# Performance work log

Measured on AMD Instinct MI355X. Metric: run time of the kernel, lower is better.

## Reference

```python
import jax, jax.numpy as jnp
import numpy as np

NMS_THRESH = 0.4          # used as both iou_threshold and score_threshold (as in source)
VAR0, VAR1 = 0.1, 0.2     # variances
MAX_OUT = 200             # max_output_size hardcoded in source
N_ANCHORS = 172032        # 2*(256^2+128^2+64^2), strides 8/16/32 on 2048x2048


def _decode(cls_pred, reg_pred, lnd_pred, anchors):
    # scores: prob of face class (column 1)
    scores = cls_pred.reshape(-1, 2)[:, 1]
    reg = reg_pred.reshape(-1, 4) * jnp.array([VAR0, VAR0, VAR1, VAR1], dtype=reg_pred.dtype)
    dx, dy, dw, dh = reg[:, 0], reg[:, 1], reg[:, 2], reg[:, 3]
    x_a, y_a, w_a, h_a = anchors[:, 0], anchors[:, 1], anchors[:, 2], anchors[:, 3]
    xc = dx * w_a + x_a
    yc = dy * h_a + y_a
    w = jnp.exp(dw) * w_a
    h = jnp.exp(dh) * h_a
    # boxes in [ymin, xmin, ymax, xmax] (tf.image.non_max_suppression convention)
    boxes = jnp.stack([yc - h / 2, xc - w / 2, yc + h / 2, xc + w / 2], axis=1)
    lnd = lnd_pred.reshape(-1, 5, 2) * VAR0
    lx = lnd[..., 0] * w_a[:, None] + x_a[:, None]
    ly = lnd[..., 1] * h_a[:, None] + y_a[:, None]
    lnd10 = jnp.stack([lx, ly], axis=-1).reshape(-1, 10)
    return boxes, scores, lnd10


def _nms(boxes, scores):
    # Greedy NMS, fixed MAX_OUT iterations; invalid slots flagged False.
    y1, x1, y2, x2 = boxes[:, 0], boxes[:, 1], boxes[:, 2], boxes[:, 3]
    areas = (y2 - y1) * (x2 - x1)
    s0 = jnp.where(scores > NMS_THRESH, scores, -jnp.inf)  # score_threshold

    def step(s, _):
        i = jnp.argmax(s)
        valid = s[i] > -jnp.inf
        b = boxes[i]  # (4,) = [iy1, ix1, iy2, ix2]
        ih = jnp.maximum(jnp.minimum(y2, b[2]) - jnp.maximum(y1, b[0]), 0.0)
        iw = jnp.maximum(jnp.minimum(x2, b[3]) - jnp.maximum(x1, b[1]), 0.0)
        inter = ih * iw
        iou = inter / (areas + areas[i] - inter + 1e-12)
        # selected box has IoU 1 with itself -> suppressed too
        s = jnp.where(valid & (iou > NMS_THRESH), -jnp.inf, s)
        return s, (i, valid)

    _, (idxs, valids) = jax.lax.scan(step, s0, None, length=MAX_OUT)
    return idxs, valids


def setup_inputs() -> dict:
    key = jax.random.key(0)
    k1, k2, k3, k4 = jax.random.split(key, 4)
    N = N_ANCHORS
    cls_pred = jax.random.normal(k1, (N, 2), jnp.float32)
    reg_pred = jax.random.normal(k2, (N, 4), jnp.float32) * 0.5
    lnd_pred = jax.random.normal(k3, (N, 10), jnp.float32) * 0.5
    centers = jax.random.uniform(k4, (N, 2), jnp.float32)  # normalized anchor centers
    wh = jnp.full((N, 2), 0.05, jnp.float32)               # anchor widths/heights
    anchors = jnp.concatenate([centers, wh], axis=1)       # [N,4] = (xc, yc, w, h)
    return {"cls_pred": cls_pred, "reg_pred": reg_pred, "lnd_pred": lnd_pred, "anchors": anchors}


def reference(cls_pred, reg_pred, lnd_pred, anchors):
    boxes, scores, lnd10 = _decode(cls_pred, reg_pred, lnd_pred, anchors)
    idxs, valids = _nms(boxes, scores)
    m = valids.astype(boxes.dtype)[:, None]
    # fixed-shape padded outputs: invalid rows zeroed (tf returns variable length)
    return boxes[idxs] * m, lnd10[idxs] * m
```

## Files before the change

kernel.cpp:

```cpp
#include <hip/hip_runtime.h>
#include <stdint.h>

#pragma clang fp contract(off)

#define N_ANCHORS 172032
#define MAX_OUT 200
#define BLK 1024
#define GRID 168
#define NW (BLK / 64)
#define SEG 32
#define NKEY (GRID * SEG)
#define RMAX 1024
#define MASKW (RMAX / 64)
#define MBLK 256
#define MROWS 16
#define RCAND 64
#define RGRID (NKEY / RCAND)
#define RBLK 512
#define RW (RBLK / 64)
#define VT 2.35f

typedef unsigned long long ull;
static_assert(GRID * BLK == N_ANCHORS, "grid covers anchors exactly");
static_assert(RMAX % 64 == 0, "mask words");
static_assert(RGRID * RCAND == NKEY, "rank grid covers key capacity");
static_assert(GRID <= 192, "prefix scan uses 3 waves");

__device__ __forceinline__ void decode_box_d(const float4* __restrict__ reg,
                                             const float4* __restrict__ anc, int i,
                                             double b[4]) {
#pragma clang fp contract(off)
    float4 r = reg[i];
    float4 a = anc[i];
    double dx = (double)r.x * 0.1;
    double dy = (double)r.y * 0.1;
    double dw = (double)r.z * 0.2;
    double dh = (double)r.w * 0.2;
    double xa = (double)a.x, ya = (double)a.y, wa = (double)a.z, ha = (double)a.w;
    double xc = dx * wa; xc = xc + xa;
    double yc = dy * ha; yc = yc + ya;
    double w = exp(dw) * wa;
    double h = exp(dh) * ha;
    double h2 = h * 0.5, w2 = w * 0.5;
    b[0] = yc - h2; b[1] = xc - w2; b[2] = yc + h2; b[3] = xc + w2;
}

__device__ __forceinline__ void write_row(const float4* __restrict__ reg,
                                          const float4* __restrict__ anc,
                                          const float* __restrict__ lnd,
                                          int q, int idx, float* __restrict__ out) {
#pragma clang fp contract(off)
    float b[4] = {0.f, 0.f, 0.f, 0.f};
    float l10[10] = {0.f, 0.f, 0.f, 0.f, 0.f, 0.f, 0.f, 0.f, 0.f, 0.f};
    if (idx >= 0) {
        double bb[4];
        decode_box_d(reg, anc, idx, bb);
        b[0] = (float)bb[0]; b[1] = (float)bb[1]; b[2] = (float)bb[2]; b[3] = (float)bb[3];
        float4 a = anc[idx];
        double xa = (double)a.x, ya = (double)a.y, wa = (double)a.z, ha = (double)a.w;
        for (int j = 0; j < 5; ++j) {
            double lx = (double)lnd[idx * 10 + 2 * j]     * 0.1;
            double ly = (double)lnd[idx * 10 + 2 * j + 1] * 0.1;
            lx = lx * wa; lx = lx + xa;
            ly = ly * ha; ly = ly + ya;
            l10[2 * j] = (float)lx; l10[2 * j + 1] = (float)ly;
        }
    }
    for (int c = 0; c < 4; ++c)  out[q * 4 + c] = b[c];
    for (int c = 0; c < 10; ++c) out[MAX_OUT * 4 + q * 10 + c] = l10[c];
}

__device__ __forceinline__ ull wmax(ull k) {
    for (int d = 32; d > 0; d >>= 1) {
        ull o = __shfl_down(k, d, 64);
        if (o > k) k = o;
    }
    return k;
}

__device__ __forceinline__ ull readlane64(ull v, int l) {
    unsigned lo = (unsigned)__builtin_amdgcn_readlane((int)(unsigned)(v & 0xffffffffull), l);
    unsigned hi = (unsigned)__builtin_amdgcn_readlane((int)(unsigned)(v >> 32), l);
    return ((ull)hi << 32) | (ull)lo;
}

__device__ __forceinline__ bool iou_gt_f4(float4 a, float4 p) {
#pragma clang fp contract(off)
    double y1 = (double)a.x, x1 = (double)a.y, y2 = (double)a.z, x2 = (double)a.w;
    double p0 = (double)p.x, p1 = (double)p.y, p2 = (double)p.z, p3 = (double)p.w;
    double ih = fmin(y2, p2) - fmax(y1, p0); ih = fmax(ih, 0.0);
    double iw = fmin(x2, p3) - fmax(x1, p1); iw = fmax(iw, 0.0);
    double inter = ih * iw;
    double aj = (y2 - y1) * (x2 - x1);
    double ap = (p2 - p0) * (p3 - p1);
    double den = aj + ap; den = den - inter; den = den + 1e-12;
    return (inter / den) > 0.4;
}

__global__ void __launch_bounds__(BLK) k_seg(const float2* __restrict__ cls,
                                             int* __restrict__ segcnt,
                                             ull* __restrict__ segkeys) {
    __shared__ int wcnt[NW];
    int tid = threadIdx.x, bid = blockIdx.x;
    int i = bid * BLK + tid;
    float sc = cls[i].y;
    bool c = (sc > VT);
    ull key = 0ull;
    if (c) key = ((ull)__float_as_uint(sc) << 32)
               | (ull)(0xFFFFFFFFu - (unsigned int)i);
    ull m = __ballot(c);
    int wid = tid >> 6, lane = tid & 63;
    if (lane == 0) wcnt[wid] = __popcll(m);
    __syncthreads();
    if (tid == 0) {
        int s = 0;
        for (int w = 0; w < NW; ++w) { int t = wcnt[w]; wcnt[w] = s; s += t; }
        segcnt[bid] = s;
    }
    __syncthreads();
    if (c) {
        int pos = wcnt[wid] + __popcll(m & ((1ull << lane) - 1ull));
        if (pos < SEG) segkeys[bid * SEG + pos] = key;
    }
}

__device__ __forceinline__ void rank_emit(const float4* __restrict__ reg,
                                          const float4* __restrict__ anc,
                                          int rank, ull key,
                                          int* __restrict__ gidx,
                                          float4* __restrict__ gbox) {
    int idx = (int)(0xFFFFFFFFu - (unsigned int)key);
    gidx[rank] = idx;
    double b[4];
    decode_box_d(reg, anc, idx, b);
    gbox[rank] = make_float4((float)b[0], (float)b[1], (float)b[2], (float)b[3]);
}

__global__ void __launch_bounds__(RBLK) k_rank(const float4* __restrict__ reg,
                                               const float4* __restrict__ anc,
                                               const int* __restrict__ segcnt,
                                               const ull* __restrict__ segkeys,
                                               int* __restrict__ meta,
                                               int* __restrict__ gidx,
                                               float4* __restrict__ gbox) {
    __shared__ ull skeys[NKEY];
    __shared__ int scnt[GRID], spre[GRID];
    __shared__ int wsum[4];
    __shared__ ull wovf[4];
    __shared__ int spart[RBLK];
    __shared__ int s_ok, s_csel;
    int tid = threadIdx.x, wid = tid >> 6, lane = tid & 63;

    int v = 0; bool ovf = false;
    if (tid < GRID) { v = segcnt[tid]; scnt[tid] = v; ovf = (v > SEG); }
    int x = v;
    for (int d = 1; d < 64; d <<= 1) {
        int o = __shfl_up(x, d, 64);
        if (lane >= d) x += o;
    }
    ull om = __ballot(ovf);
    if (wid < 3 && lane == 63) { wsum[wid] = x; wovf[wid] = om; }
    __syncthreads();
    if (tid == 0) {
        int total = wsum[0] + wsum[1] + wsum[2];
        s_csel = total;
        s_ok = ((wovf[0] | wovf[1] | wovf[2]) == 0ull) ? 1 : 0;
        if (blockIdx.x == 0) { meta[0] = s_ok; meta[1] = total; }
    }
    __syncthreads();
    if (tid < GRID)
        spre[tid] = (x - v) + (wid >= 1 ? wsum[0] : 0) + (wid >= 2 ? wsum[1] : 0);
    bool okl = (s_ok != 0);
    int csel = s_csel;
    int cbase = blockIdx.x * RCAND;
    __syncthreads();
    if (!okl) return;
    if (cbase >= csel) return;

    for (int t = tid; t < GRID * SEG; t += RBLK) {
        int s = t >> 5, k = t & (SEG - 1);
        if (k < scnt[s]) skeys[spre[s] + k] = segkeys[t];
    }
    __syncthreads();

    int per = (csel + RW - 1) / RW;
    int jb = wid * per;
    int je = jb + per; if (je > csel) je = csel;
    int c = cbase + lane;
    ull kc = (c < csel) ? skeys[c] : 0ull;
    int rk = 0;
#pragma unroll 8
    for (int j = jb; j < je; ++j)
        rk += (skeys[j] > kc) ? 1 : 0;
    spart[wid * 64 + lane] = rk;
    __syncthreads();

    if (tid < RCAND) {
        int cc = cbase + tid;
        if (cc < csel) {
            int r = 0;
#pragma unroll
            for (int w = 0; w < RW; ++w) r += spart[w * 64 + tid];
            if (r < RMAX) rank_emit(reg, anc, r, skeys[cc], gidx, gbox);
        }
    }
}

__global__ void __launch_bounds__(MBLK) k_mask(const int* __restrict__ meta,
                                               const float4* __restrict__ gbox,
                                               ull* __restrict__ gmask) {
    __shared__ float4 cbox[RMAX];
    if (meta[0] == 0) return;
    int csel = meta[1];
    int rlim = csel < RMAX ? csel : RMAX;
    int tid = threadIdx.x;
    for (int t = tid; t < RMAX; t += MBLK) cbox[t] = gbox[t];
    __syncthreads();
    int row  = blockIdx.x * MROWS + (tid & (MROWS - 1));
    int word = tid >> 4;
    if (row >= rlim) return;
    float4 br = cbox[row];
    ull bits = 0ull;
    int cbase = word << 6;
#pragma unroll 4
    for (int e = 0; e < 64; ++e) {
        int c = cbase + e;
        if (c < rlim && iou_gt_f4(cbox[c], br)) bits |= (1ull << e);
    }
    gmask[row * MASKW + word] = bits;
}

__global__ void __launch_bounds__(BLK) k_pick(const float2* __restrict__ cls,
                                              const float4* __restrict__ reg,
                                              const float4* __restrict__ anc,
                                              const float* __restrict__ lnd,
                                              const int* __restrict__ meta,
                                              const int* __restrict__ gidx,
                                              const ull* __restrict__ gmask,
                                              float* __restrict__ sbuf,
                                              float* __restrict__ out) {
    __shared__ __align__(16) ull smask[RMAX * MASKW];
    __shared__ int s_kept[MAX_OUT];
    __shared__ int s_ln;
    __shared__ ull warr[NW];
    __shared__ ull s_win;
    __shared__ double s_pb[5];

    int tid = threadIdx.x;
    bool pre_ok = (meta[0] != 0);
    int csel = meta[1];
    int ln = 0;

    if (pre_ok) {
        int rlim = csel < RMAX ? csel : RMAX;
        int nv4 = rlim * (MASKW / 2);
        const float4* gm4 = (const float4*)gmask;
        float4* sm4 = (float4*)smask;
        for (int t = tid; t < nv4; t += BLK) sm4[t] = gm4[t];
        __syncthreads();
        if (tid < 64) {
            int lane = tid;
            ull alive = 0ull;
            if (lane < MASKW) {
                int lo = lane << 6;
                int n = rlim - lo;
                if (n >= 64) alive = ~0ull;
                else if (n > 0) alive = (1ull << n) - 1ull;
            }
            int lnl = 0;
            while (lnl < MAX_OUT) {
                ull bal = __ballot(alive != 0ull);
                if (bal == 0ull) break;
                int wl = __ffsll(bal) - 1;
                ull aw = readlane64(alive, wl);
                int bit = __ffsll(aw) - 1;
                int p = (wl << 6) + bit;
                if (lane == 0) s_kept[lnl] = p;
                lnl++;
                ull rw = (lane < MASKW) ? smask[p * MASKW + lane] : 0ull;
                alive &= ~rw;
            }
            if (lane == 0) s_ln = lnl;
        }
        __syncthreads();
        ln = s_ln;
    }

    bool need = (!pre_ok) || (ln < MAX_OUT);
    if (!need) {
        if (tid < MAX_OUT) write_row(reg, anc, lnd, tid, gidx[s_kept[tid]], out);
        return;
    }

    for (int i = tid; i < N_ANCHORS; i += BLK) {
        float sc = cls[i].y;
        sbuf[i] = ((double)sc > 0.4) ? sc : 0.0f;
    }
    __syncthreads();
    ln = 0;
    for (int oi = 0; oi < MAX_OUT; ++oi) {
        ull k = 0;
        for (int i = tid; i < N_ANCHORS; i += BLK) {
            ull kk = ((ull)__float_as_uint(sbuf[i]) << 32)
                   | (ull)(0xFFFFFFFFu - (unsigned int)i);
            if (kk > k) k = kk;
        }
        k = wmax(k);
        if ((tid & 63) == 0) warr[tid >> 6] = k;
        __syncthreads();
        if (tid < 64) {
            ull v = (tid < NW) ? warr[tid] : 0ull;
            v = wmax(v);
            if (tid == 0) s_win = v;
        }
        __syncthreads();
        ull win = s_win;
        if ((win >> 32) == 0u) break;
        int pidx = (int)(0xFFFFFFFFu - (unsigned int)win);
        if (tid == 0) {
            double b[4];
            decode_box_d(reg, anc, pidx, b);
            s_pb[0] = b[0]; s_pb[1] = b[1]; s_pb[2] = b[2]; s_pb[3] = b[3];
            s_pb[4] = (b[2] - b[0]) * (b[3] - b[1]);
            s_kept[oi] = pidx;
        }
        __syncthreads();
        double p0 = s_pb[0], p1 = s_pb[1], p2 = s_pb[2], p3 = s_pb[3], pa = s_pb[4];
        for (int i = tid; i < N_ANCHORS; i += BLK) {
            float v = sbuf[i];
            if (v != 0.0f) {
                double b[4];
                decode_box_d(reg, anc, i, b);
                double ih = fmin(b[2], p2) - fmax(b[0], p0); ih = fmax(ih, 0.0);
                double iw = fmin(b[3], p3) - fmax(b[1], p1); iw = fmax(iw, 0.0);
                double inter = ih * iw;
                double aa = (b[2] - b[0]) * (b[3] - b[1]);
                double den = aa + pa; den = den - inter; den = den + 1e-12;
                if (inter / den > 0.4) sbuf[i] = 0.0f;
            }
        }
        __syncthreads();
        ln = oi + 1;
    }
    __syncthreads();
    if (tid < MAX_OUT)
        write_row(reg, anc, lnd, tid, (tid < ln) ? s_kept[tid] : -1, out);
}

extern "C" void kernel_launch(void* const* d_in, const int* in_sizes, int n_in,
                              void* d_out, int out_size, void* d_ws, size_t ws_size,
                              hipStream_t stream) {
    const float2* cls = (const float2*)d_in[0];
    const float4* reg = (const float4*)d_in[1];
    const float*  lnd = (const float*)d_in[2];
    const float4* anc = (const float4*)d_in[3];

    uint8_t* w = (uint8_t*)d_ws;
    int*    segcnt  = (int*)w;
    int*    meta    = (int*)(w + 768);
    ull*    segkeys = (ull*)(w + 1024);
    int*    gidx    = (int*)(w + 44032);
    float4* gbox    = (float4*)(w + 48128);
    ull*    gmask   = (ull*)(w + 64512);
    float*  sbuf    = (float*)(w + 44032);

    k_seg <<<GRID, BLK, 0, stream>>>(cls, segcnt, segkeys);
    k_rank<<<RGRID, RBLK, 0, stream>>>(reg, anc, segcnt, segkeys, meta, gidx, gbox);
    k_mask<<<RMAX / MROWS, MBLK, 0, stream>>>(meta, gbox, gmask);
    k_pick<<<1, BLK, 0, stream>>>(cls, reg, anc, lnd, meta, gidx, gmask, sbuf,
                                  (float*)d_out);
}
```

Measured before the change: 116.2 us.

## Fuse four NMS kernels into one cooperative kernel with grid syncs

New measurement: 292.7 us. 152% more time.

```diff
diff --git a/kernel.cpp b/kernel.cpp
--- a/kernel.cpp
+++ b/kernel.cpp
@@ -1,5 +1,8 @@
 #include <hip/hip_runtime.h>
+#include <hip/hip_cooperative_groups.h>
 #include <stdint.h>
+
+namespace cg = cooperative_groups;
 
 #pragma clang fp contract(off)
 
@@ -12,18 +15,14 @@
 #define NKEY (GRID * SEG)
 #define RMAX 1024
 #define MASKW (RMAX / 64)
-#define MBLK 256
-#define MROWS 16
-#define RCAND 64
-#define RGRID (NKEY / RCAND)
-#define RBLK 512
-#define RW (RBLK / 64)
+#define RCAND 32
+#define NSLICE 32
 #define VT 2.35f
 
 typedef unsigned long long ull;
 static_assert(GRID * BLK == N_ANCHORS, "grid covers anchors exactly");
 static_assert(RMAX % 64 == 0, "mask words");
-static_assert(RGRID * RCAND == NKEY, "rank grid covers key capacity");
+static_assert(GRID * RCAND == NKEY, "rank grid covers key capacity");
 static_assert(GRID <= 192, "prefix scan uses 3 waves");
 
 __device__ __forceinline__ void decode_box_d(const float4* __restrict__ reg,
@@ -50,24 +49,28 @@
                                           const float* __restrict__ lnd,
                                           int q, int idx, float* __restrict__ out) {
 #pragma clang fp contract(off)
-    float b[4] = {0.f, 0.f, 0.f, 0.f};
-    float l10[10] = {0.f, 0.f, 0.f, 0.f, 0.f, 0.f, 0.f, 0.f, 0.f, 0.f};
+    float4 bv = make_float4(0.f, 0.f, 0.f, 0.f);
+    float2 lv[5];
+    for (int j = 0; j < 5; ++j) lv[j] = make_float2(0.f, 0.f);
     if (idx >= 0) {
         double bb[4];
         decode_box_d(reg, anc, idx, bb);
-        b[0] = (float)bb[0]; b[1] = (float)bb[1]; b[2] = (float)bb[2]; b[3] = (float)bb[3];
+        bv = make_float4((float)bb[0], (float)bb[1], (float)bb[2], (float)bb[3]);
         float4 a = anc[idx];
         double xa = (double)a.x, ya = (double)a.y, wa = (double)a.z, ha = (double)a.w;
+        const float2* l2p = (const float2*)lnd;
         for (int j = 0; j < 5; ++j) {
-            double lx = (double)lnd[idx * 10 + 2 * j]     * 0.1;
-            double ly = (double)lnd[idx * 10 + 2 * j + 1] * 0.1;
+            float2 lp = l2p[idx * 5 + j];
+            double lx = (double)lp.x * 0.1;
+            double ly = (double)lp.y * 0.1;
             lx = lx * wa; lx = lx + xa;
             ly = ly * ha; ly = ly + ya;
-            l10[2 * j] = (float)lx; l10[2 * j + 1] = (float)ly;
-        }
-    }
-    for (int c = 0; c < 4; ++c)  out[q * 4 + c] = b[c];
-    for (int c = 0; c < 10; ++c) out[MAX_OUT * 4 + q * 10 + c] = l10[c];
+            lv[j] = make_float2((float)lx, (float)ly);
+        }
+    }
+    *(float4*)&out[q * 4] = bv;
+    float2* o2 = (float2*)&out[MAX_OUT * 4 + q * 10];
+    for (int j = 0; j < 5; ++j) o2[j] = lv[j];
 }
 
 __device__ __forceinline__ ull wmax(ull k) {
@@ -97,33 +100,6 @@
     return (inter / den) > 0.4;
 }
 
-__global__ void __launch_bounds__(BLK) k_seg(const float2* __restrict__ cls,
-                                             int* __restrict__ segcnt,
-                                             ull* __restrict__ segkeys) {
-    __shared__ int wcnt[NW];
-    int tid = threadIdx.x, bid = blockIdx.x;
-    int i = bid * BLK + tid;
-    float sc = cls[i].y;
-    bool c = (sc > VT);
-    ull key = 0ull;
-    if (c) key = ((ull)__float_as_uint(sc) << 32)
-               | (ull)(0xFFFFFFFFu - (unsigned int)i);
-    ull m = __ballot(c);
-    int wid = tid >> 6, lane = tid & 63;
-    if (lane == 0) wcnt[wid] = __popcll(m);
-    __syncthreads();
-    if (tid == 0) {
-        int s = 0;
-        for (int w = 0; w < NW; ++w) { int t = wcnt[w]; wcnt[w] = s; s += t; }
-        segcnt[bid] = s;
-    }
-    __syncthreads();
-    if (c) {
-        int pos = wcnt[wid] + __popcll(m & ((1ull << lane) - 1ull));
-        if (pos < SEG) segkeys[bid * SEG + pos] = key;
-    }
-}
-
 __device__ __forceinline__ void rank_emit(const float4* __restrict__ reg,
                                           const float4* __restrict__ anc,
                                           int rank, ull key,
@@ -136,130 +112,158 @@
     gbox[rank] = make_float4((float)b[0], (float)b[1], (float)b[2], (float)b[3]);
 }
 
-__global__ void __launch_bounds__(RBLK) k_rank(const float4* __restrict__ reg,
-                                               const float4* __restrict__ anc,
-                                               const int* __restrict__ segcnt,
-                                               const ull* __restrict__ segkeys,
-                                               int* __restrict__ meta,
-                                               int* __restrict__ gidx,
-                                               float4* __restrict__ gbox) {
-    __shared__ ull skeys[NKEY];
-    __shared__ int scnt[GRID], spre[GRID];
-    __shared__ int wsum[4];
-    __shared__ ull wovf[4];
-    __shared__ int spart[RBLK];
-    __shared__ int s_ok, s_csel;
-    int tid = threadIdx.x, wid = tid >> 6, lane = tid & 63;
-
-    int v = 0; bool ovf = false;
-    if (tid < GRID) { v = segcnt[tid]; scnt[tid] = v; ovf = (v > SEG); }
-    int x = v;
-    for (int d = 1; d < 64; d <<= 1) {
-        int o = __shfl_up(x, d, 64);
-        if (lane >= d) x += o;
-    }
-    ull om = __ballot(ovf);
-    if (wid < 3 && lane == 63) { wsum[wid] = x; wovf[wid] = om; }
-    __syncthreads();
-    if (tid == 0) {
-        int total = wsum[0] + wsum[1] + wsum[2];
-        s_csel = total;
-        s_ok = ((wovf[0] | wovf[1] | wovf[2]) == 0ull) ? 1 : 0;
-        if (blockIdx.x == 0) { meta[0] = s_ok; meta[1] = total; }
-    }
-    __syncthreads();
-    if (tid < GRID)
-        spre[tid] = (x - v) + (wid >= 1 ? wsum[0] : 0) + (wid >= 2 ? wsum[1] : 0);
-    bool okl = (s_ok != 0);
-    int csel = s_csel;
-    int cbase = blockIdx.x * RCAND;
-    __syncthreads();
-    if (!okl) return;
-    if (cbase >= csel) return;
-
-    for (int t = tid; t < GRID * SEG; t += RBLK) {
-        int s = t >> 5, k = t & (SEG - 1);
-        if (k < scnt[s]) skeys[spre[s] + k] = segkeys[t];
-    }
-    __syncthreads();
-
-    int per = (csel + RW - 1) / RW;
-    int jb = wid * per;
-    int je = jb + per; if (je > csel) je = csel;
-    int c = cbase + lane;
-    ull kc = (c < csel) ? skeys[c] : 0ull;
-    int rk = 0;
+union Smem {
+    int wcnt[NW];
+    struct {
+        ull skeys[NKEY];
+        int scnt[GRID];
+        int spre[GRID];
+        int spart[NSLICE * RCAND];
+        int wsum[4];
+        ull wovf[4];
+        int ok, csel;
+    } b;
+    float4 cbox[RMAX];
+    struct {
+        ull smask[RMAX * MASKW];
+        int s_kept[MAX_OUT];
+        int s_ln;
+        ull warr[NW];
+        ull s_win;
+        double s_pb[5];
+    } d;
+};
+
+__global__ void __launch_bounds__(BLK) k_all(const float2* __restrict__ cls,
+                                             const float4* __restrict__ reg,
+                                             const float4* __restrict__ anc,
+                                             const float* __restrict__ lnd,
+                                             int* __restrict__ segcnt,
+                                             ull* __restrict__ segkeys,
+                                             int* __restrict__ gidx,
+                                             float4* __restrict__ gbox,
+                                             ull* __restrict__ gmask,
+                                             float* __restrict__ sbuf,
+                                             float* __restrict__ out) {
+    cg::grid_group grid = cg::this_grid();
+    __shared__ Smem sm;
+    int tid = threadIdx.x, bid = blockIdx.x;
+    int wid = tid >> 6, lane = tid & 63;
+
+    {
+        int i = bid * BLK + tid;
+        float sc = cls[i].y;
+        bool c = (sc > VT);
+        ull key = 0ull;
+        if (c) key = ((ull)__float_as_uint(sc) << 32)
+                   | (ull)(0xFFFFFFFFu - (unsigned int)i);
+        ull m = __ballot(c);
+        if (lane == 0) sm.wcnt[wid] = __popcll(m);
+        __syncthreads();
+        if (tid == 0) {
+            int s = 0;
+            for (int w = 0; w < NW; ++w) { int t = sm.wcnt[w]; sm.wcnt[w] = s; s += t; }
+            segcnt[bid] = s;
+        }
+        __syncthreads();
+        if (c) {
+            int pos = sm.wcnt[wid] + __popcll(m & ((1ull << lane) - 1ull));
+            if (pos < SEG) segkeys[bid * SEG + pos] = key;
+        }
+        __syncthreads();
+    }
+    __threadfence();
+    grid.sync();
+
+    int ok, csel;
+    {
+        int v = 0; bool ovf = false;
+        if (tid < GRID) { v = segcnt[tid]; sm.b.scnt[tid] = v; ovf = (v > SEG); }
+        int x = v;
+        for (int d = 1; d < 64; d <<= 1) {
+            int o = __shfl_up(x, d, 64);
+            if (lane >= d) x += o;
+        }
+        ull om = __ballot(ovf);
+        if (wid < 3 && lane == 63) { sm.b.wsum[wid] = x; sm.b.wovf[wid] = om; }
+        __syncthreads();
+        if (tid == 0) {
+            sm.b.csel = sm.b.wsum[0] + sm.b.wsum[1] + sm.b.wsum[2];
+            sm.b.ok = ((sm.b.wovf[0] | sm.b.wovf[1] | sm.b.wovf[2]) == 0ull) ? 1 : 0;
+        }
+        __syncthreads();
+        if (tid < GRID)
+            sm.b.spre[tid] = (x - v) + (wid >= 1 ? sm.b.wsum[0] : 0)
+                                     + (wid >= 2 ? sm.b.wsum[1] : 0);
+        ok = sm.b.ok; csel = sm.b.csel;
+        __syncthreads();
+
+        int cbase = bid * RCAND;
+        bool active = (ok != 0) && (cbase < csel);
+        if (active) {
+            for (int t = tid; t < GRID * SEG; t += BLK) {
+                int s = t >> 5, k = t & (SEG - 1);
+                if (k < sm.b.scnt[s]) sm.b.skeys[sm.b.spre[s] + k] = segkeys[t];
+            }
+        }
+        __syncthreads();
+        if (active) {
+            int cand = lane & (RCAND - 1);
+            int sl = (wid << 1) | (lane >> 5);
+            int per = (csel + NSLICE - 1) / NSLICE;
+            int jb = sl * per, je = jb + per; if (je > csel) je = csel;
+            int cc = cbase + cand;
+            ull kc = (cc < csel) ? sm.b.skeys[cc] : 0ull;
+            int rk = 0;
 #pragma unroll 8
-    for (int j = jb; j < je; ++j)
-        rk += (skeys[j] > kc) ? 1 : 0;
-    spart[wid * 64 + lane] = rk;
-    __syncthreads();
-
-    if (tid < RCAND) {
-        int cc = cbase + tid;
-        if (cc < csel) {
-            int r = 0;
+            for (int j = jb; j < je; ++j)
+                rk += (sm.b.skeys[j] > kc) ? 1 : 0;
+            sm.b.spart[sl * RCAND + cand] = rk;
+        }
+        __syncthreads();
+        if (active && tid < RCAND) {
+            int cc = cbase + tid;
+            if (cc < csel) {
+                int r = 0;
 #pragma unroll
-            for (int w = 0; w < RW; ++w) r += spart[w * 64 + tid];
-            if (r < RMAX) rank_emit(reg, anc, r, skeys[cc], gidx, gbox);
-        }
-    }
-}
-
-__global__ void __launch_bounds__(MBLK) k_mask(const int* __restrict__ meta,
-                                               const float4* __restrict__ gbox,
-                                               ull* __restrict__ gmask) {
-    __shared__ float4 cbox[RMAX];
-    if (meta[0] == 0) return;
-    int csel = meta[1];
+                for (int s = 0; s < NSLICE; ++s) r += sm.b.spart[s * RCAND + tid];
+                if (r < RMAX) rank_emit(reg, anc, r, sm.b.skeys[cc], gidx, gbox);
+            }
+        }
+        __syncthreads();
+    }
+    __threadfence();
+    grid.sync();
+
     int rlim = csel < RMAX ? csel : RMAX;
-    int tid = threadIdx.x;
-    for (int t = tid; t < RMAX; t += MBLK) cbox[t] = gbox[t];
-    __syncthreads();
-    int row  = blockIdx.x * MROWS + (tid & (MROWS - 1));
-    int word = tid >> 4;
-    if (row >= rlim) return;
-    float4 br = cbox[row];
-    ull bits = 0ull;
-    int cbase = word << 6;
-#pragma unroll 4
-    for (int e = 0; e < 64; ++e) {
-        int c = cbase + e;
-        if (c < rlim && iou_gt_f4(cbox[c], br)) bits |= (1ull << e);
-    }
-    gmask[row * MASKW + word] = bits;
-}
-
-__global__ void __launch_bounds__(BLK) k_pick(const float2* __restrict__ cls,
-                                              const float4* __restrict__ reg,
-                                              const float4* __restrict__ anc,
-                                              const float* __restrict__ lnd,
-                                              const int* __restrict__ meta,
-                                              const int* __restrict__ gidx,
-                                              const ull* __restrict__ gmask,
-                                              float* __restrict__ sbuf,
-                                              float* __restrict__ out) {
-    __shared__ __align__(16) ull smask[RMAX * MASKW];
-    __shared__ int s_kept[MAX_OUT];
-    __shared__ int s_ln;
-    __shared__ ull warr[NW];
-    __shared__ ull s_win;
-    __shared__ double s_pb[5];
-
-    int tid = threadIdx.x;
-    bool pre_ok = (meta[0] != 0);
-    int csel = meta[1];
+    if (ok && rlim > 0) {
+        for (int t = tid; t < rlim; t += BLK) sm.cbox[t] = gbox[t];
+        __syncthreads();
+        int gw = bid * NW + wid;
+        int totw = rlim * MASKW;
+        for (int w = gw; w < totw; w += GRID * NW) {
+            int row = w >> 4, word = w & (MASKW - 1);
+            int col = (word << 6) + lane;
+            bool hit = (col < rlim) && iou_gt_f4(sm.cbox[col], sm.cbox[row]);
+            ull bits = __ballot(hit);
+            if (lane == 0) gmask[w] = bits;
+        }
+        __syncthreads();
+    }
+    __threadfence();
+    grid.sync();
+
+    if (bid != 0) return;
+
     int ln = 0;
-
+    bool pre_ok = (ok != 0);
     if (pre_ok) {
-        int rlim = csel < RMAX ? csel : RMAX;
         int nv4 = rlim * (MASKW / 2);
         const float4* gm4 = (const float4*)gmask;
-        float4* sm4 = (float4*)smask;
+        float4* sm4 = (float4*)sm.d.smask;
         for (int t = tid; t < nv4; t += BLK) sm4[t] = gm4[t];
         __syncthreads();
         if (tid < 64) {
-            int lane = tid;
             ull alive = 0ull;
             if (lane < MASKW) {
                 int lo = lane << 6;
@@ -275,20 +279,20 @@
                 ull aw = readlane64(alive, wl);
                 int bit = __ffsll(aw) - 1;
                 int p = (wl << 6) + bit;
-                if (lane == 0) s_kept[lnl] = p;
+                if (lane == 0) sm.d.s_kept[lnl] = p;
                 lnl++;
-                ull rw = (lane < MASKW) ? smask[p * MASKW + lane] : 0ull;
+                ull rw = (lane < MASKW) ? sm.d.smask[p * MASKW + lane] : 0ull;
                 alive &= ~rw;
             }
-            if (lane == 0) s_ln = lnl;
-        }
-        __syncthreads();
-        ln = s_ln;
+            if (lane == 0) sm.d.s_ln = lnl;
+        }
+        __syncthreads();
+        ln = sm.d.s_ln;
     }
 
     bool need = (!pre_ok) || (ln < MAX_OUT);
     if (!need) {
-        if (tid < MAX_OUT) write_row(reg, anc, lnd, tid, gidx[s_kept[tid]], out);
+        if (tid < MAX_OUT) write_row(reg, anc, lnd, tid, gidx[sm.d.s_kept[tid]], out);
         return;
     }
 
@@ -306,26 +310,28 @@
             if (kk > k) k = kk;
         }
         k = wmax(k);
-        if ((tid & 63) == 0) warr[tid >> 6] = k;
+        if ((tid & 63) == 0) sm.d.warr[tid >> 6] = k;
         __syncthreads();
         if (tid < 64) {
-            ull v = (tid < NW) ? warr[tid] : 0ull;
+            ull v = (tid < NW) ? sm.d.warr[tid] : 0ull;
             v = wmax(v);
-            if (tid == 0) s_win = v;
-        }
-        __syncthreads();
-        ull win = s_win;
+            if (tid == 0) sm.d.s_win = v;
+        }
+        __syncthreads();
+        ull win = sm.d.s_win;
         if ((win >> 32) == 0u) break;
         int pidx = (int)(0xFFFFFFFFu - (unsigned int)win);
         if (tid == 0) {
             double b[4];
             decode_box_d(reg, anc, pidx, b);
-            s_pb[0] = b[0]; s_pb[1] = b[1]; s_pb[2] = b[2]; s_pb[3] = b[3];
-            s_pb[4] = (b[2] - b[0]) * (b[3] - b[1]);
-            s_kept[oi] = pidx;
-        }
-        __syncthreads();
-        double p0 = s_pb[0], p1 = s_pb[1], p2 = s_pb[2], p3 = s_pb[3], pa = s_pb[4];
+            sm.d.s_pb[0] = b[0]; sm.d.s_pb[1] = b[1]; sm.d.s_pb[2] = b[2];
+            sm.d.s_pb[3] = b[3];
+            sm.d.s_pb[4] = (b[2] - b[0]) * (b[3] - b[1]);
+            sm.d.s_kept[oi] = pidx;
+        }
+        __syncthreads();
+        double p0 = sm.d.s_pb[0], p1 = sm.d.s_pb[1], p2 = sm.d.s_pb[2],
+               p3 = sm.d.s_pb[3], pa = sm.d.s_pb[4];
         for (int i = tid; i < N_ANCHORS; i += BLK) {
             float v = sbuf[i];
             if (v != 0.0f) {
@@ -344,7 +350,7 @@
     }
     __syncthreads();
     if (tid < MAX_OUT)
-        write_row(reg, anc, lnd, tid, (tid < ln) ? s_kept[tid] : -1, out);
+        write_row(reg, anc, lnd, tid, (tid < ln) ? sm.d.s_kept[tid] : -1, out);
 }
 
 extern "C" void kernel_launch(void* const* d_in, const int* in_sizes, int n_in,
@@ -357,16 +363,16 @@
 
     uint8_t* w = (uint8_t*)d_ws;
     int*    segcnt  = (int*)w;
-    int*    meta    = (int*)(w + 768);
     ull*    segkeys = (ull*)(w + 1024);
     int*    gidx    = (int*)(w + 44032);
     float4* gbox    = (float4*)(w + 48128);
     ull*    gmask   = (ull*)(w + 64512);
     float*  sbuf    = (float*)(w + 44032);
-
-    k_seg <<<GRID, BLK, 0, stream>>>(cls, segcnt, segkeys);
-    k_rank<<<RGRID, RBLK, 0, stream>>>(reg, anc, segcnt, segkeys, meta, gidx, gbox);
-    k_mask<<<RMAX / MROWS, MBLK, 0, stream>>>(meta, gbox, gmask);
-    k_pick<<<1, BLK, 0, stream>>>(cls, reg, anc, lnd, meta, gidx, gmask, sbuf,
-                                  (float*)d_out);
-}
+    float*  outp    = (float*)d_out;
+
+    void* args[] = {(void*)&cls, (void*)&reg, (void*)&anc, (void*)&lnd,
+                    (void*)&segcnt, (void*)&segkeys, (void*)&gidx, (void*)&gbox,
+                    (void*)&gmask, (void*)&sbuf, (void*)&outp};
+    hipLaunchCooperativeKernel((const void*)k_all, dim3(GRID), dim3(BLK),
+                               args, 0, stream);
+}
```

## Fuse IoU mask and greedy pick kernels via last-block atomic handoff

Applied to the files above, without the earlier changes.

After: 115.7 us. Within noise of the previous version (-0.4%).

```diff
diff --git a/kernel.cpp b/kernel.cpp
--- a/kernel.cpp
+++ b/kernel.cpp
@@ -12,12 +12,11 @@
 #define NKEY (GRID * SEG)
 #define RMAX 1024
 #define MASKW (RMAX / 64)
-#define MBLK 256
-#define MROWS 16
 #define RCAND 64
 #define RGRID (NKEY / RCAND)
 #define RBLK 512
 #define RW (RBLK / 64)
+#define MGRID 64
 #define VT 2.35f
 
 typedef unsigned long long ull;
@@ -50,24 +49,28 @@
                                           const float* __restrict__ lnd,
                                           int q, int idx, float* __restrict__ out) {
 #pragma clang fp contract(off)
-    float b[4] = {0.f, 0.f, 0.f, 0.f};
-    float l10[10] = {0.f, 0.f, 0.f, 0.f, 0.f, 0.f, 0.f, 0.f, 0.f, 0.f};
+    float4 bv = make_float4(0.f, 0.f, 0.f, 0.f);
+    float2 lv[5];
+    for (int j = 0; j < 5; ++j) lv[j] = make_float2(0.f, 0.f);
     if (idx >= 0) {
         double bb[4];
         decode_box_d(reg, anc, idx, bb);
-        b[0] = (float)bb[0]; b[1] = (float)bb[1]; b[2] = (float)bb[2]; b[3] = (float)bb[3];
+        bv = make_float4((float)bb[0], (float)bb[1], (float)bb[2], (float)bb[3]);
         float4 a = anc[idx];
         double xa = (double)a.x, ya = (double)a.y, wa = (double)a.z, ha = (double)a.w;
+        const float2* l2p = (const float2*)lnd;
         for (int j = 0; j < 5; ++j) {
-            double lx = (double)lnd[idx * 10 + 2 * j]     * 0.1;
-            double ly = (double)lnd[idx * 10 + 2 * j + 1] * 0.1;
+            float2 lp = l2p[idx * 5 + j];
+            double lx = (double)lp.x * 0.1;
+            double ly = (double)lp.y * 0.1;
             lx = lx * wa; lx = lx + xa;
             ly = ly * ha; ly = ly + ya;
-            l10[2 * j] = (float)lx; l10[2 * j + 1] = (float)ly;
-        }
-    }
-    for (int c = 0; c < 4; ++c)  out[q * 4 + c] = b[c];
-    for (int c = 0; c < 10; ++c) out[MAX_OUT * 4 + q * 10 + c] = l10[c];
+            lv[j] = make_float2((float)lx, (float)ly);
+        }
+    }
+    *(float4*)&out[q * 4] = bv;
+    float2* o2 = (float2*)&out[MAX_OUT * 4 + q * 10];
+    for (int j = 0; j < 5; ++j) o2[j] = lv[j];
 }
 
 __device__ __forceinline__ ull wmax(ull k) {
@@ -99,9 +102,11 @@
 
 __global__ void __launch_bounds__(BLK) k_seg(const float2* __restrict__ cls,
                                              int* __restrict__ segcnt,
-                                             ull* __restrict__ segkeys) {
+                                             ull* __restrict__ segkeys,
+                                             int* __restrict__ cnt) {
     __shared__ int wcnt[NW];
     int tid = threadIdx.x, bid = blockIdx.x;
+    if (bid == 0 && tid == 0) cnt[0] = 0;
     int i = bid * BLK + tid;
     float sc = cls[i].y;
     bool c = (sc > VT);
@@ -206,60 +211,63 @@
     }
 }
 
-__global__ void __launch_bounds__(MBLK) k_mask(const int* __restrict__ meta,
-                                               const float4* __restrict__ gbox,
-                                               ull* __restrict__ gmask) {
-    __shared__ float4 cbox[RMAX];
-    if (meta[0] == 0) return;
-    int csel = meta[1];
-    int rlim = csel < RMAX ? csel : RMAX;
-    int tid = threadIdx.x;
-    for (int t = tid; t < RMAX; t += MBLK) cbox[t] = gbox[t];
-    __syncthreads();
-    int row  = blockIdx.x * MROWS + (tid & (MROWS - 1));
-    int word = tid >> 4;
-    if (row >= rlim) return;
-    float4 br = cbox[row];
-    ull bits = 0ull;
-    int cbase = word << 6;
-#pragma unroll 4
-    for (int e = 0; e < 64; ++e) {
-        int c = cbase + e;
-        if (c < rlim && iou_gt_f4(cbox[c], br)) bits |= (1ull << e);
-    }
-    gmask[row * MASKW + word] = bits;
-}
-
-__global__ void __launch_bounds__(BLK) k_pick(const float2* __restrict__ cls,
-                                              const float4* __restrict__ reg,
-                                              const float4* __restrict__ anc,
-                                              const float* __restrict__ lnd,
-                                              const int* __restrict__ meta,
-                                              const int* __restrict__ gidx,
-                                              const ull* __restrict__ gmask,
-                                              float* __restrict__ sbuf,
-                                              float* __restrict__ out) {
-    __shared__ __align__(16) ull smask[RMAX * MASKW];
+__global__ void __launch_bounds__(BLK) k_mp(const float2* __restrict__ cls,
+                                            const float4* __restrict__ reg,
+                                            const float4* __restrict__ anc,
+                                            const float* __restrict__ lnd,
+                                            const int* __restrict__ meta,
+                                            const int* __restrict__ gidx,
+                                            const float4* __restrict__ gbox,
+                                            ull* __restrict__ gmask,
+                                            int* __restrict__ cnt,
+                                            float* __restrict__ sbuf,
+                                            float* __restrict__ out) {
+    __shared__ union {
+        float4 cbox[RMAX];
+        __align__(16) ull smask[RMAX * MASKW];
+    } u;
     __shared__ int s_kept[MAX_OUT];
-    __shared__ int s_ln;
+    __shared__ int s_ln, s_last;
     __shared__ ull warr[NW];
     __shared__ ull s_win;
     __shared__ double s_pb[5];
 
-    int tid = threadIdx.x;
+    int tid = threadIdx.x, bid = blockIdx.x;
+    int wid = tid >> 6, lane = tid & 63;
     bool pre_ok = (meta[0] != 0);
     int csel = meta[1];
+    int rlim = csel < RMAX ? csel : RMAX;
+
+    if (pre_ok && rlim > 0) {
+        for (int t = tid; t < rlim; t += BLK) u.cbox[t] = gbox[t];
+        __syncthreads();
+        int totw = rlim * MASKW;
+        for (int w = bid * NW + wid; w < totw; w += MGRID * NW) {
+            int row = w >> 4, word = w & (MASKW - 1);
+            int col = (word << 6) + lane;
+            bool hit = (col < rlim) && iou_gt_f4(u.cbox[col], u.cbox[row]);
+            ull bits = __ballot(hit);
+            if (lane == 0) gmask[w] = bits;
+        }
+    }
+    __syncthreads();
+    if (tid == 0) {
+        __threadfence();
+        int prev = atomicAdd(cnt, 1);
+        s_last = (prev == MGRID - 1) ? 1 : 0;
+    }
+    __syncthreads();
+    if (!s_last) return;
+    __threadfence();
+
     int ln = 0;
-
     if (pre_ok) {
-        int rlim = csel < RMAX ? csel : RMAX;
         int nv4 = rlim * (MASKW / 2);
         const float4* gm4 = (const float4*)gmask;
-        float4* sm4 = (float4*)smask;
+        float4* sm4 = (float4*)u.smask;
         for (int t = tid; t < nv4; t += BLK) sm4[t] = gm4[t];
         __syncthreads();
         if (tid < 64) {
-            int lane = tid;
             ull alive = 0ull;
             if (lane < MASKW) {
                 int lo = lane << 6;
@@ -277,7 +285,7 @@
                 int p = (wl << 6) + bit;
                 if (lane == 0) s_kept[lnl] = p;
                 lnl++;
-                ull rw = (lane < MASKW) ? smask[p * MASKW + lane] : 0ull;
+                ull rw = (lane < MASKW) ? u.smask[p * MASKW + lane] : 0ull;
                 alive &= ~rw;
             }
             if (lane == 0) s_ln = lnl;
@@ -358,15 +366,15 @@
     uint8_t* w = (uint8_t*)d_ws;
     int*    segcnt  = (int*)w;
     int*    meta    = (int*)(w + 768);
+    int*    cnt     = (int*)(w + 896);
     ull*    segkeys = (ull*)(w + 1024);
     int*    gidx    = (int*)(w + 44032);
     float4* gbox    = (float4*)(w + 48128);
     ull*    gmask   = (ull*)(w + 64512);
     float*  sbuf    = (float*)(w + 44032);
 
-    k_seg <<<GRID, BLK, 0, stream>>>(cls, segcnt, segkeys);
+    k_seg <<<GRID, BLK, 0, stream>>>(cls, segcnt, segkeys, cnt);
     k_rank<<<RGRID, RBLK, 0, stream>>>(reg, anc, segcnt, segkeys, meta, gidx, gbox);
-    k_mask<<<RMAX / MROWS, MBLK, 0, stream>>>(meta, gbox, gmask);
-    k_pick<<<1, BLK, 0, stream>>>(cls, reg, anc, lnd, meta, gidx, gmask, sbuf,
-                                  (float*)d_out);
-}
+    k_mp  <<<MGRID, BLK, 0, stream>>>(cls, reg, anc, lnd, meta, gidx, gbox, gmask,
+                                      cnt, sbuf, (float*)d_out);
+}
```
